# Kernel tuning notes

Measured on AMD Instinct MI355X. Metric: run time of the kernel, lower is better.

## Reference

```python
import jax, jax.numpy as jnp
import numpy as np
from math import sqrt

SCALE = sqrt(512.0)  # max(key_size, attn_hidden_size, query_size) with scaled=True

def setup_inputs() -> dict:
    key = jax.random.key(0)
    k1, k2, k3, k4, k5 = jax.random.split(key, 5)
    B, T, S, M, N, H = 8, 512, 512, 512, 512, 128
    return {
        "query": jax.random.normal(k1, (B, T, M), dtype=jnp.float32),
        "keys": jax.random.normal(k2, (B, S, N), dtype=jnp.float32),
        "W1": jax.random.normal(k3, (N, H), dtype=jnp.float32),
        "W2": jax.random.normal(k4, (M, H), dtype=jnp.float32),
        "v": jax.random.normal(k5, (H,), dtype=jnp.float32),
    }

def reference(query, keys, W1, W2, v):
    # Project query and keys into attention hidden space
    x1 = jnp.einsum('btm,mh->bth', query, W2)   # (B,T,H)
    x2 = jnp.einsum('bsn,nh->bsh', keys, W1)    # (B,S,H)
    # Broadcast merge (op='add'), tanh activation, v-weighted reduction over H
    merged = jnp.tanh(x1[:, :, None, :] + x2[:, None, :, :])  # (B,T,S,H)
    score = jnp.einsum('btsh,h->bts', merged, v)
    return score / SCALE
```

## Files before the change

kernel.cpp:

```cpp
#include <hip/hip_runtime.h>
#include <hip/hip_fp16.h>


typedef float vf2 __attribute__((ext_vector_type(2)));

constexpr float SCALE_IN  = 2.8853900817779268f;
constexpr float INV_SCALE = 0.04419417382415922f;

__global__ __launch_bounds__(256) void proj_kernel(
    const float* __restrict__ q,  const float* __restrict__ w2,
    const float* __restrict__ ky, const float* __restrict__ w1,
    unsigned int* __restrict__ x1w, unsigned int* __restrict__ x2w) {
  __shared__ float As[16 * 64];
  __shared__ float Ws[64 * 128];

  int blk = blockIdx.x;
  const float* A; const float* W; unsigned int* O;
  if (blk < 256) { A = q;  W = w2; O = x1w; }
  else           { blk -= 256; A = ky; W = w1; O = x2w; }
  const int rbase = blk * 16;
  const int tid = threadIdx.x;
  const int hq  = tid & 31;
  const int rg  = tid >> 5;

  float acc[2][4];
#pragma unroll
  for (int r = 0; r < 2; ++r)
#pragma unroll
    for (int c = 0; c < 4; ++c) acc[r][c] = 0.0f;

  for (int kb = 0; kb < 512; kb += 64) {
    {
      const int arow = tid >> 4;
      const int k4   = (tid & 15) * 4;
      *(float4*)(As + arow * 64 + k4) =
          *(const float4*)(A + (size_t)(rbase + arow) * 512 + kb + k4);
      const int hq4 = (tid & 31) * 4;
      const int w0  = tid >> 5;
#pragma unroll
      for (int p = 0; p < 8; ++p)
        *(float4*)(Ws + (w0 + 8 * p) * 128 + hq4) =
            *(const float4*)(W + (size_t)(kb + w0 + 8 * p) * 128 + hq4);
    }
    __syncthreads();
#pragma unroll 4
    for (int k4 = 0; k4 < 64; k4 += 4) {
      float a[2][4], w[4][4];
      *(float4*)a[0] = *(const float4*)(As + (2 * rg + 0) * 64 + k4);
      *(float4*)a[1] = *(const float4*)(As + (2 * rg + 1) * 64 + k4);
#pragma unroll
      for (int kk = 0; kk < 4; ++kk)
        *(float4*)w[kk] = *(const float4*)(Ws + (k4 + kk) * 128 + 4 * hq);
#pragma unroll
      for (int kk = 0; kk < 4; ++kk)
#pragma unroll
        for (int r = 0; r < 2; ++r)
#pragma unroll
          for (int c = 0; c < 4; ++c)
            acc[r][c] = fmaf(a[r][kk], w[kk][c], acc[r][c]);
    }
    __syncthreads();
  }

#pragma unroll
  for (int r = 0; r < 2; ++r) {
    unsigned int pk[4];
#pragma unroll
    for (int c = 0; c < 4; ++c) {
      const float z  = acc[r][c] * SCALE_IN;
      const float kf = rintf(z);
      const int   ki = (int)kf;
      const float em = __builtin_amdgcn_exp2f(z - kf);
      pk[c] = ((unsigned int)ki << 16) |
              (unsigned int)__half_as_ushort(__float2half_rn(em));
    }
    *(uint4*)(O + (size_t)(rbase + 2 * rg + r) * 128 + 4 * hq) = *(uint4*)pk;
  }
}

__global__ __launch_bounds__(256) void score_kernel(
    const unsigned int* __restrict__ x1w, const unsigned int* __restrict__ x2w,
    const float* __restrict__ v, float* __restrict__ out) {
  __shared__ unsigned int x1l[64 * 64];
  __shared__ unsigned int x2l[64 * 32];

  const int tid   = threadIdx.x;
  const int b     = blockIdx.x >> 7;
  const int tile  = blockIdx.x & 127;
  const int tbase = (tile >> 4) * 64;
  const int sbase = (tile & 15) * 32;

  const int sg = tid & 15;
  const int tg = tid >> 4;

  const int st_t = tid >> 2, st_q = tid & 3;
  const int s2_t = tid >> 3, s2_q = tid & 7;

  const uint4* x1g = (const uint4*)x1w + (size_t)(b * 512 + tbase) * 32;
  const uint4* x2g = (const uint4*)x2w + (size_t)(b * 512 + sbase) * 32;

  vf2 racc[4];
#pragma unroll
  for (int i = 0; i < 4; ++i) racc[i] = (vf2){0.0f, 0.0f};
  float sv = 0.0f;

  for (int c = 0; c < 2; ++c) {
    if (c) __syncthreads();
#pragma unroll
    for (int p = 0; p < 4; ++p) {
      const int hq = st_q + 4 * p;
      const uint4 a = x1g[(size_t)st_t * 32 + 16 * c + hq];
      x1l[(4 * hq + 0) * 64 + st_t] = a.x;
      x1l[(4 * hq + 1) * 64 + st_t] = a.y;
      x1l[(4 * hq + 2) * 64 + st_t] = a.z;
      x1l[(4 * hq + 3) * 64 + st_t] = a.w;
    }
#pragma unroll
    for (int p = 0; p < 2; ++p) {
      const int hq = s2_q + 8 * p;
      const uint4 a = x2g[(size_t)s2_t * 32 + 16 * c + hq];
      x2l[(4 * hq + 0) * 32 + s2_t] = a.x;
      x2l[(4 * hq + 1) * 32 + s2_t] = a.y;
      x2l[(4 * hq + 2) * 32 + s2_t] = a.z;
      x2l[(4 * hq + 3) * 32 + s2_t] = a.w;
    }
    __syncthreads();

    for (int hg = 0; hg < 16; ++hg) {
      const int h0 = 4 * hg;
      const float4 vq = *(const float4*)(v + 64 * c + h0);
      sv += (vq.x + vq.y) + (vq.z + vq.w);

      float emt[4][4]; int kt[4][4];
      vf2 ems[4]; int ks[4][2];
#pragma unroll
      for (int qq = 0; qq < 4; ++qq) {
        const uint4 tp = *(const uint4*)(x1l + (h0 + qq) * 64 + 4 * tg);
        emt[qq][0] = __half2float(__ushort_as_half((unsigned short)tp.x));
        kt [qq][0] = ((int)tp.x) >> 16;
        emt[qq][1] = __half2float(__ushort_as_half((unsigned short)tp.y));
        kt [qq][1] = ((int)tp.y) >> 16;
        emt[qq][2] = __half2float(__ushort_as_half((unsigned short)tp.z));
        kt [qq][2] = ((int)tp.z) >> 16;
        emt[qq][3] = __half2float(__ushort_as_half((unsigned short)tp.w));
        kt [qq][3] = ((int)tp.w) >> 16;
        const uint2 sp = *(const uint2*)(x2l + (h0 + qq) * 32 + 2 * sg);
        ems[qq].x = __half2float(__ushort_as_half((unsigned short)sp.x));
        ems[qq].y = __half2float(__ushort_as_half((unsigned short)sp.y));
        ks [qq][0] = ((int)sp.x) >> 16;
        ks [qq][1] = ((int)sp.y) >> 16;
      }

#pragma unroll
      for (int i = 0; i < 4; ++i) {
        vf2 Aq[4];
#pragma unroll
        for (int qq = 0; qq < 4; ++qq) {
          const int k0 = min(kt[qq][i] + ks[qq][0], 30);
          const int k1 = min(kt[qq][i] + ks[qq][1], 30);
          const vf2 m = emt[qq][i] * ems[qq];
          vf2 e; e.x = ldexpf(m.x, k0); e.y = ldexpf(m.y, k1);
          Aq[qq] = e + 1.0f;
        }
        const vf2 N01 = vq.x * Aq[1] + vq.y * Aq[0];
        const vf2 N23 = vq.z * Aq[3] + vq.w * Aq[2];
        const vf2 D01 = Aq[0] * Aq[1];
        const vf2 D23 = Aq[2] * Aq[3];
        const vf2 NUM = N01 * D23 + N23 * D01;
        const vf2 DEN = D01 * D23;
        vf2 R;
        R.x = __builtin_amdgcn_rcpf(DEN.x);
        R.y = __builtin_amdgcn_rcpf(DEN.y);
        racc[i] += NUM * R;
      }
    }
  }

  const float c1 = sv * INV_SCALE;
  const float c2 = -2.0f * INV_SCALE;
#pragma unroll
  for (int i = 0; i < 4; ++i) {
    const vf2 o = c2 * racc[i] + c1;
    *(vf2*)(out + (size_t)(b * 512 + tbase + 4 * tg + i) * 512 + sbase + 2 * sg) = o;
  }
}

extern "C" void kernel_launch(void* const* d_in, const int* in_sizes, int n_in,
                              void* d_out, int out_size, void* d_ws, size_t ws_size,
                              hipStream_t stream) {
  const float* query = (const float*)d_in[0];
  const float* keys  = (const float*)d_in[1];
  const float* W1    = (const float*)d_in[2];
  const float* W2    = (const float*)d_in[3];
  const float* v     = (const float*)d_in[4];
  float* out = (float*)d_out;

  unsigned int* x1w = (unsigned int*)d_ws;
  unsigned int* x2w = x1w + 8 * 512 * 128;

  hipLaunchKernelGGL(proj_kernel, dim3(512), dim3(256), 0, stream,
                     query, W2, keys, W1, x1w, x2w);
  hipLaunchKernelGGL(score_kernel, dim3(1024), dim3(256), 0, stream,
                     x1w, x2w, v, out);
}
```

Measured before the change: 145.7 us.

## Store exp2 projections as floats and batch 8-term rational tanh reduction

The projection kernel now writes clamped exp2(x/4) as a plain float instead of a packed exponent plus half-precision mantissa. The score kernel can then form 1+e^(x1+x2) from a multiply, a square, a clamp and an FMA, which removes the integer unpacking and the ldexp calls. Score terms are combined in groups of 8 over H, so there is one reciprocal per 8 terms instead of per 4. Both kernels also gain register prefetch of the next LDS tile, padded LDS rows and occupancy hints. The trade-off is more LDS traffic from the float layout, plus reliance on the clamp keeping the 8-term product of denominators below float overflow.

```diff
diff --git a/kernel.cpp b/kernel.cpp
--- a/kernel.cpp
+++ b/kernel.cpp
@@ -1,27 +1,38 @@
 #include <hip/hip_runtime.h>
-#include <hip/hip_fp16.h>
 
 
 typedef float vf2 __attribute__((ext_vector_type(2)));
 
 constexpr float SCALE_IN  = 2.8853900817779268f;
 constexpr float INV_SCALE = 0.04419417382415922f;
-
-__global__ __launch_bounds__(256) void proj_kernel(
+constexpr float CLAMP_HI  = 181.01933598375617f;
+
+__global__ __launch_bounds__(256, 2) void proj_kernel(
     const float* __restrict__ q,  const float* __restrict__ w2,
     const float* __restrict__ ky, const float* __restrict__ w1,
-    unsigned int* __restrict__ x1w, unsigned int* __restrict__ x2w) {
-  __shared__ float As[16 * 64];
+    float* __restrict__ x1q, float* __restrict__ x2q) {
+  __shared__ float As[16 * 68];
   __shared__ float Ws[64 * 128];
 
   int blk = blockIdx.x;
-  const float* A; const float* W; unsigned int* O;
-  if (blk < 256) { A = q;  W = w2; O = x1w; }
-  else           { blk -= 256; A = ky; W = w1; O = x2w; }
+  const float* A; const float* W; float* O;
+  if (blk < 256) { A = q;  W = w2; O = x1q; }
+  else { blk -= 256; A = ky; W = w1; O = x2q; }
   const int rbase = blk * 16;
   const int tid = threadIdx.x;
-  const int hq  = tid & 31;
-  const int rg  = tid >> 5;
+
+  const int arow = tid >> 4, ak = (tid & 15) * 4;
+  const int wrow = tid >> 5, wh = (tid & 31) * 4;
+  const int rg = tid >> 5;
+  const int hq = (tid & 31) * 4;
+
+  const float* Ab = A + (size_t)(rbase + arow) * 512 + ak;
+  const float* Wb = W + (size_t)wrow * 128 + wh;
+
+  float4 pa, pw[8];
+  pa = *(const float4*)Ab;
+#pragma unroll
+  for (int p = 0; p < 8; ++p) pw[p] = *(const float4*)(Wb + (size_t)(8 * p) * 128);
 
   float acc[2][4];
 #pragma unroll
@@ -29,60 +40,57 @@
 #pragma unroll
     for (int c = 0; c < 4; ++c) acc[r][c] = 0.0f;
 
-  for (int kb = 0; kb < 512; kb += 64) {
-    {
-      const int arow = tid >> 4;
-      const int k4   = (tid & 15) * 4;
-      *(float4*)(As + arow * 64 + k4) =
-          *(const float4*)(A + (size_t)(rbase + arow) * 512 + kb + k4);
-      const int hq4 = (tid & 31) * 4;
-      const int w0  = tid >> 5;
+  for (int c = 0; c < 8; ++c) {
+    __syncthreads();
+    *(float4*)(As + arow * 68 + ak) = pa;
+#pragma unroll
+    for (int p = 0; p < 8; ++p)
+      *(float4*)(Ws + (wrow + 8 * p) * 128 + wh) = pw[p];
+    __syncthreads();
+    if (c < 7) {
+      const int kb = 64 * (c + 1);
+      pa = *(const float4*)(Ab + kb);
 #pragma unroll
       for (int p = 0; p < 8; ++p)
-        *(float4*)(Ws + (w0 + 8 * p) * 128 + hq4) =
-            *(const float4*)(W + (size_t)(kb + w0 + 8 * p) * 128 + hq4);
-    }
-    __syncthreads();
+        pw[p] = *(const float4*)(Wb + (size_t)(kb + 8 * p) * 128);
+    }
 #pragma unroll 4
     for (int k4 = 0; k4 < 64; k4 += 4) {
-      float a[2][4], w[4][4];
-      *(float4*)a[0] = *(const float4*)(As + (2 * rg + 0) * 64 + k4);
-      *(float4*)a[1] = *(const float4*)(As + (2 * rg + 1) * 64 + k4);
+      float a0[4], a1[4], w[4][4];
+      *(float4*)a0 = *(const float4*)(As + (2 * rg + 0) * 68 + k4);
+      *(float4*)a1 = *(const float4*)(As + (2 * rg + 1) * 68 + k4);
 #pragma unroll
       for (int kk = 0; kk < 4; ++kk)
-        *(float4*)w[kk] = *(const float4*)(Ws + (k4 + kk) * 128 + 4 * hq);
+        *(float4*)w[kk] = *(const float4*)(Ws + (k4 + kk) * 128 + hq);
 #pragma unroll
       for (int kk = 0; kk < 4; ++kk)
 #pragma unroll
-        for (int r = 0; r < 2; ++r)
-#pragma unroll
-          for (int c = 0; c < 4; ++c)
-            acc[r][c] = fmaf(a[r][kk], w[kk][c], acc[r][c]);
-    }
-    __syncthreads();
+        for (int cc = 0; cc < 4; ++cc) {
+          acc[0][cc] = fmaf(a0[kk], w[kk][cc], acc[0][cc]);
+          acc[1][cc] = fmaf(a1[kk], w[kk][cc], acc[1][cc]);
+        }
+    }
   }
 
 #pragma unroll
   for (int r = 0; r < 2; ++r) {
-    unsigned int pk[4];
-#pragma unroll
-    for (int c = 0; c < 4; ++c) {
-      const float z  = acc[r][c] * SCALE_IN;
-      const float kf = rintf(z);
-      const int   ki = (int)kf;
-      const float em = __builtin_amdgcn_exp2f(z - kf);
-      pk[c] = ((unsigned int)ki << 16) |
-              (unsigned int)__half_as_ushort(__float2half_rn(em));
-    }
-    *(uint4*)(O + (size_t)(rbase + 2 * rg + r) * 128 + 4 * hq) = *(uint4*)pk;
+    float4 o;
+    float* op = (float*)&o;
+#pragma unroll
+    for (int cc = 0; cc < 4; ++cc) {
+      float zq = acc[r][cc] * (SCALE_IN * 0.25f);
+      zq = __builtin_amdgcn_fmed3f(zq, -126.0f, 126.0f);
+      op[cc] = __builtin_amdgcn_exp2f(zq);
+    }
+    *(float4*)(O + (size_t)(rbase + 2 * rg + r) * 128 + hq) = o;
   }
 }
 
-__global__ __launch_bounds__(256) void score_kernel(
-    const unsigned int* __restrict__ x1w, const unsigned int* __restrict__ x2w,
+__global__ __launch_bounds__(256, 4) void score_kernel(
+    const float* __restrict__ x1q, const float* __restrict__ x2q,
     const float* __restrict__ v, float* __restrict__ out) {
-  __shared__ unsigned int x1l[64 * 64];
-  __shared__ unsigned int x2l[64 * 32];
+  __shared__ float x1l[32 * 68];
+  __shared__ float x2l[32 * 34];
 
   const int tid   = threadIdx.x;
   const int b     = blockIdx.x >> 7;
@@ -93,85 +101,89 @@
   const int sg = tid & 15;
   const int tg = tid >> 4;
 
-  const int st_t = tid >> 2, st_q = tid & 3;
-  const int s2_t = tid >> 3, s2_q = tid & 7;
-
-  const uint4* x1g = (const uint4*)x1w + (size_t)(b * 512 + tbase) * 32;
-  const uint4* x2g = (const uint4*)x2w + (size_t)(b * 512 + sbase) * 32;
-
-  vf2 racc[4];
-#pragma unroll
-  for (int i = 0; i < 4; ++i) racc[i] = (vf2){0.0f, 0.0f};
+  const int t1 = tid >> 2, f1 = tid & 3;
+  const int s2 = tid >> 3, f2 = tid & 7;
+
+  const float* x1g = x1q + (size_t)(b * 512 + tbase + t1) * 128;
+  const float* x2g = x2q + (size_t)(b * 512 + sbase + s2) * 128;
+
   float sv = 0.0f;
-
-  for (int c = 0; c < 2; ++c) {
-    if (c) __syncthreads();
-#pragma unroll
-    for (int p = 0; p < 4; ++p) {
-      const int hq = st_q + 4 * p;
-      const uint4 a = x1g[(size_t)st_t * 32 + 16 * c + hq];
-      x1l[(4 * hq + 0) * 64 + st_t] = a.x;
-      x1l[(4 * hq + 1) * 64 + st_t] = a.y;
-      x1l[(4 * hq + 2) * 64 + st_t] = a.z;
-      x1l[(4 * hq + 3) * 64 + st_t] = a.w;
-    }
-#pragma unroll
-    for (int p = 0; p < 2; ++p) {
-      const int hq = s2_q + 8 * p;
-      const uint4 a = x2g[(size_t)s2_t * 32 + 16 * c + hq];
-      x2l[(4 * hq + 0) * 32 + s2_t] = a.x;
-      x2l[(4 * hq + 1) * 32 + s2_t] = a.y;
-      x2l[(4 * hq + 2) * 32 + s2_t] = a.z;
-      x2l[(4 * hq + 3) * 32 + s2_t] = a.w;
-    }
-    __syncthreads();
-
-    for (int hg = 0; hg < 16; ++hg) {
-      const int h0 = 4 * hg;
-      const float4 vq = *(const float4*)(v + 64 * c + h0);
-      sv += (vq.x + vq.y) + (vq.z + vq.w);
-
-      float emt[4][4]; int kt[4][4];
-      vf2 ems[4]; int ks[4][2];
-#pragma unroll
-      for (int qq = 0; qq < 4; ++qq) {
-        const uint4 tp = *(const uint4*)(x1l + (h0 + qq) * 64 + 4 * tg);
-        emt[qq][0] = __half2float(__ushort_as_half((unsigned short)tp.x));
-        kt [qq][0] = ((int)tp.x) >> 16;
-        emt[qq][1] = __half2float(__ushort_as_half((unsigned short)tp.y));
-        kt [qq][1] = ((int)tp.y) >> 16;
-        emt[qq][2] = __half2float(__ushort_as_half((unsigned short)tp.z));
-        kt [qq][2] = ((int)tp.z) >> 16;
-        emt[qq][3] = __half2float(__ushort_as_half((unsigned short)tp.w));
-        kt [qq][3] = ((int)tp.w) >> 16;
-        const uint2 sp = *(const uint2*)(x2l + (h0 + qq) * 32 + 2 * sg);
-        ems[qq].x = __half2float(__ushort_as_half((unsigned short)sp.x));
-        ems[qq].y = __half2float(__ushort_as_half((unsigned short)sp.y));
-        ks [qq][0] = ((int)sp.x) >> 16;
-        ks [qq][1] = ((int)sp.y) >> 16;
+  for (int i = 0; i < 128; i += 4) {
+    const float4 vx = *(const float4*)(v + i);
+    sv += (vx.x + vx.y) + (vx.z + vx.w);
+  }
+
+  float racc[4][2];
+#pragma unroll
+  for (int i = 0; i < 4; ++i) { racc[i][0] = 0.0f; racc[i][1] = 0.0f; }
+
+  float4 pa0, pa1, pb;
+  pa0 = *(const float4*)(x1g + 4 * f1);
+  pa1 = *(const float4*)(x1g + 16 + 4 * f1);
+  pb  = *(const float4*)(x2g + 4 * f2);
+
+  for (int c = 0; c < 4; ++c) {
+    __syncthreads();
+    {
+      const float* s4 = (const float*)&pa0;
+      const float* s5 = (const float*)&pa1;
+#pragma unroll
+      for (int j = 0; j < 4; ++j) {
+        x1l[(4 * f1 + j) * 68 + t1]        = s4[j];
+        x1l[(16 + 4 * f1 + j) * 68 + t1]   = s5[j];
       }
+      const float* s6 = (const float*)&pb;
+#pragma unroll
+      for (int j = 0; j < 4; ++j)
+        x2l[(4 * f2 + j) * 34 + s2] = s6[j];
+    }
+    __syncthreads();
+    if (c < 3) {
+      const int hb = 32 * (c + 1);
+      pa0 = *(const float4*)(x1g + hb + 4 * f1);
+      pa1 = *(const float4*)(x1g + hb + 16 + 4 * f1);
+      pb  = *(const float4*)(x2g + hb + 4 * f2);
+    }
+
+#pragma unroll
+    for (int hg = 0; hg < 4; ++hg) {
+      const int h0 = 8 * hg;
+      float qt[8][4]; float qs[8][2]; float vh[8];
+#pragma unroll
+      for (int qq = 0; qq < 8; ++qq) {
+        *(float4*)qt[qq] = *(const float4*)(x1l + (h0 + qq) * 68 + 4 * tg);
+        *(vf2*)qs[qq]    = *(const vf2*)(x2l + (h0 + qq) * 34 + 2 * sg);
+        vh[qq] = v[32 * c + h0 + qq];
+      }
 
 #pragma unroll
       for (int i = 0; i < 4; ++i) {
-        vf2 Aq[4];
-#pragma unroll
-        for (int qq = 0; qq < 4; ++qq) {
-          const int k0 = min(kt[qq][i] + ks[qq][0], 30);
-          const int k1 = min(kt[qq][i] + ks[qq][1], 30);
-          const vf2 m = emt[qq][i] * ems[qq];
-          vf2 e; e.x = ldexpf(m.x, k0); e.y = ldexpf(m.y, k1);
-          Aq[qq] = e + 1.0f;
+#pragma unroll
+        for (int j = 0; j < 2; ++j) {
+          float A[8];
+#pragma unroll
+          for (int qq = 0; qq < 8; ++qq) {
+            const float p  = qt[qq][i] * qs[qq][j];
+            const float pp = p * p;
+            const float cc = __builtin_amdgcn_fmed3f(pp, 0.0f, CLAMP_HI);
+            A[qq] = fmaf(cc, cc, 1.0f);
+          }
+          const float n01 = fmaf(vh[1], A[0], vh[0] * A[1]);
+          const float d01 = A[0] * A[1];
+          const float n23 = fmaf(vh[3], A[2], vh[2] * A[3]);
+          const float d23 = A[2] * A[3];
+          const float n45 = fmaf(vh[5], A[4], vh[4] * A[5]);
+          const float d45 = A[4] * A[5];
+          const float n67 = fmaf(vh[7], A[6], vh[6] * A[7]);
+          const float d67 = A[6] * A[7];
+          const float n03 = fmaf(n23, d01, n01 * d23);
+          const float d03 = d01 * d23;
+          const float n47 = fmaf(n67, d45, n45 * d67);
+          const float d47 = d45 * d67;
+          const float num = fmaf(n47, d03, n03 * d47);
+          const float den = d03 * d47;
+          racc[i][j] = fmaf(num, __builtin_amdgcn_rcpf(den), racc[i][j]);
         }
-        const vf2 N01 = vq.x * Aq[1] + vq.y * Aq[0];
-        const vf2 N23 = vq.z * Aq[3] + vq.w * Aq[2];
-        const vf2 D01 = Aq[0] * Aq[1];
-        const vf2 D23 = Aq[2] * Aq[3];
-        const vf2 NUM = N01 * D23 + N23 * D01;
-        const vf2 DEN = D01 * D23;
-        vf2 R;
-        R.x = __builtin_amdgcn_rcpf(DEN.x);
-        R.y = __builtin_amdgcn_rcpf(DEN.y);
-        racc[i] += NUM * R;
       }
     }
   }
@@ -180,7 +192,9 @@
   const float c2 = -2.0f * INV_SCALE;
 #pragma unroll
   for (int i = 0; i < 4; ++i) {
-    const vf2 o = c2 * racc[i] + c1;
+    vf2 o;
+    o.x = fmaf(racc[i][0], c2, c1);
+    o.y = fmaf(racc[i][1], c2, c1);
     *(vf2*)(out + (size_t)(b * 512 + tbase + 4 * tg + i) * 512 + sbase + 2 * sg) = o;
   }
 }
@@ -195,11 +209,11 @@
   const float* v     = (const float*)d_in[4];
   float* out = (float*)d_out;
 
-  unsigned int* x1w = (unsigned int*)d_ws;
-  unsigned int* x2w = x1w + 8 * 512 * 128;
+  float* x1q = (float*)d_ws;
+  float* x2q = x1q + 8 * 512 * 128;
 
   hipLaunchKernelGGL(proj_kernel, dim3(512), dim3(256), 0, stream,
-                     query, W2, keys, W1, x1w, x2w);
+                     query, W2, keys, W1, x1q, x2q);
   hipLaunchKernelGGL(score_kernel, dim3(1024), dim3(256), 0, stream,
-                     x1w, x2w, v, out);
+                     x1q, x2q, v, out);
 }
```

Result: slower. 326.0 us (+123.8%).
